# Kernel optimization log

Measured on AMD Instinct MI355X. Metric: run time of the kernel, lower is better.

The kernel has to match this reference:

```python
import jax, jax.numpy as jnp
import numpy as np

KH, KW = 3, 3
C_OUT = 32


def setup_inputs() -> dict:
    key = jax.random.key(0)
    k1, k2, k3 = jax.random.split(key, 3)
    B, H, W, C_IN = 32, 128, 128, 32
    P_DIM = 128
    X = jax.random.normal(k1, (B, H, W, C_IN), dtype=jnp.float32)
    P = jax.random.normal(k2, (B, P_DIM), dtype=jnp.float32)
    # hypernetwork Dense weight: p_dim -> kh*kw*c_in*c_out (no bias, no activation)
    dense_w = jax.random.normal(k3, (P_DIM, KH * KW * C_IN * C_OUT), dtype=jnp.float32) * 0.05
    return {"X": X, "P": P, "dense_w": dense_w}


def _conv_one(x, w):
    # x: [H, W, c_in], w: [kh, kw, c_in, c_out] -> [H, W, c_out], SAME padding, stride 1
    y = jax.lax.conv_general_dilated(
        x[None], w, window_strides=(1, 1), padding="SAME",
        dimension_numbers=("NHWC", "HWIO", "NHWC"))
    return y[0]


def reference(X, P, dense_w):
    B = X.shape[0]
    c_in = X.shape[-1]
    # hypernetwork: per-sample conv kernels
    A = P @ dense_w                              # [B, kh*kw*c_in*c_out]
    Wk = A.reshape(B, KH, KW, c_in, C_OUT)       # [B, kh, kw, c_in, c_out]
    # batched per-sample conv (equivalent to tf.map_fn over conv2d)
    return jax.vmap(_conv_one)(X, Wk)            # [B, H, W, c_out]
```

## Files before the change

kernel.cpp:

```cpp
#include <hip/hip_runtime.h>


#define BATCH 32
#define HDIM 128
#define WDIM 128
#define CIN 32
#define COUT 32
#define PDIM 128
#define KCOLS 9216

typedef _Float16 f16x8 __attribute__((ext_vector_type(8)));
typedef float f32x4 __attribute__((ext_vector_type(4)));

__device__ __forceinline__ f16x8 zero8() {
    f16x8 z;
#pragma unroll
    for (int j = 0; j < 8; ++j) z[j] = (_Float16)0.f;
    return z;
}

__device__ __forceinline__ f16x8 cvt8(f32x4 lo, f32x4 hi) {
    f16x8 o;
#pragma unroll
    for (int j = 0; j < 4; ++j) {
        o[j] = (_Float16)lo[j];
        o[4 + j] = (_Float16)hi[j];
    }
    return o;
}

__global__ __launch_bounds__(256) void hyper_gemm(const float* __restrict__ P,
                                                  const float* __restrict__ Dw,
                                                  unsigned short* __restrict__ WB) {
    const int tid = threadIdx.x;
    const int lane = tid & 63;
    const int cg = blockIdx.x % 144;
    const int bq = blockIdx.x / 144;
    const int col = cg * 64 + lane;
    const int b0 = __builtin_amdgcn_readfirstlane(bq * 16 + (tid >> 6) * 4);
    const float* pb = P + (size_t)b0 * PDIM;

    float acc[4];
#pragma unroll
    for (int j = 0; j < 4; ++j) acc[j] = 0.f;

#pragma unroll 2
    for (int mm = 0; mm < PDIM; mm += 16) {
        float d[16];
#pragma unroll
        for (int u = 0; u < 16; ++u) d[u] = Dw[(size_t)(mm + u) * KCOLS + col];
#pragma unroll
        for (int u = 0; u < 16; ++u) {
#pragma unroll
            for (int j = 0; j < 4; ++j) acc[j] += d[u] * pb[j * PDIM + mm + u];
        }
    }

    const int co = col & 31;
    const int k = col >> 5;
    const int kc = k >> 5;
    const int ci = k & 31;
    const int base =
        ((kc * 2 + (co >> 4)) * 64 + (ci >> 3) * 16 + (co & 15)) * 8 + (ci & 7);
#pragma unroll
    for (int j = 0; j < 4; ++j) {
        _Float16 v = (_Float16)acc[j];
        WB[(size_t)(b0 + j) * KCOLS + base] = __builtin_bit_cast(unsigned short, v);
    }
}

__device__ __forceinline__ f16x8 halo_ld(const f32x4* __restrict__ gp, int px) {
    const bool ok = (unsigned)px < 128u;
    const int p = ok ? px : 0;
    f32x4 lo = gp[p * 8];
    f32x4 hi = gp[p * 8 + 1];
    f16x8 o;
#pragma unroll
    for (int j = 0; j < 4; ++j) {
        o[j] = (_Float16)lo[j];
        o[4 + j] = (_Float16)hi[j];
    }
    if (!ok) o = zero8();
    return o;
}

template <bool TOPG, bool PRE>
__device__ __forceinline__ void compute_group(const char* xsb, int ldsbase,
                                              const f16x8* bfl, float* ybase,
                                              const f32x4* gp, bool gvalid,
                                              int wave, int q, int m16,
                                              f32x4* R, const float* xsrc1) {
    f16x8 hal[3];
    if (gvalid) {
#pragma unroll
        for (int kw = 0; kw < 3; ++kw) hal[kw] = halo_ld(gp, m16 + kw - 1);
    } else {
#pragma unroll
        for (int kw = 0; kw < 3; ++kw) hal[kw] = zero8();
    }

    int va[3];
#pragma unroll
    for (int kw = 0; kw < 3; ++kw) {
        const int px = m16 + kw - 1;
        const int sl = (q ^ (px >> 1)) & 3;
        va[kw] = ldsbase + (wave - 1) * 8192 + px * 64 + sl * 16;
    }

#pragma unroll
    for (int t = 0; t < 8; ++t) {
        if constexpr (PRE) {
            R[2 * t] = *(const f32x4*)(xsrc1 + (size_t)t * WDIM * CIN);
            R[2 * t + 1] = *(const f32x4*)(xsrc1 + (size_t)t * WDIM * CIN + 4);
        }

        f32x4 acc0 = {0.f, 0.f, 0.f, 0.f};
        f32x4 acc1 = {0.f, 0.f, 0.f, 0.f};

#pragma unroll
        for (int kh = 0; kh < 3; ++kh) {
            f16x8 a0, a1, a2;
            const bool use_lds = (kh == 1) || (kh == 0 && (!TOPG || wave != 0)) ||
                                 (kh == 2 && wave != 7);
            if (use_lds) {
                int v0 = va[0] + kh * 8192;
                int v1 = va[1] + kh * 8192;
                int v2 = va[2] + kh * 8192;
                if (t == 0) v0 += (m16 == 0) ? 64 : 0;
                if (t == 7) v2 -= (m16 == 15) ? 64 : 0;
                a0 = *(const f16x8*)(xsb + v0);
                a1 = *(const f16x8*)(xsb + v1);
                a2 = *(const f16x8*)(xsb + v2);
                if (t == 0 && m16 == 0) a0 = zero8();
                if (t == 7 && m16 == 15) a2 = zero8();
            } else {
                a0 = hal[0];
                a1 = hal[1];
                a2 = hal[2];
                if (gvalid && t < 7) {
#pragma unroll
                    for (int kw = 0; kw < 3; ++kw)
                        hal[kw] = halo_ld(gp, (t + 1) * 16 + m16 + kw - 1);
                }
            }
            acc0 = __builtin_amdgcn_mfma_f32_16x16x32_f16(a0, bfl[((kh * 3 + 0) * 2 + 0) * 64], acc0, 0, 0, 0);
            acc1 = __builtin_amdgcn_mfma_f32_16x16x32_f16(a0, bfl[((kh * 3 + 0) * 2 + 1) * 64], acc1, 0, 0, 0);
            acc0 = __builtin_amdgcn_mfma_f32_16x16x32_f16(a1, bfl[((kh * 3 + 1) * 2 + 0) * 64], acc0, 0, 0, 0);
            acc1 = __builtin_amdgcn_mfma_f32_16x16x32_f16(a1, bfl[((kh * 3 + 1) * 2 + 1) * 64], acc1, 0, 0, 0);
            acc0 = __builtin_amdgcn_mfma_f32_16x16x32_f16(a2, bfl[((kh * 3 + 2) * 2 + 0) * 64], acc0, 0, 0, 0);
            acc1 = __builtin_amdgcn_mfma_f32_16x16x32_f16(a2, bfl[((kh * 3 + 2) * 2 + 1) * 64], acc1, 0, 0, 0);
        }

        float* yp = ybase + t * 16 * COUT;
#pragma unroll
        for (int r = 0; r < 4; ++r) {
            yp[r * COUT] = acc0[r];
            yp[r * COUT + 16] = acc1[r];
        }

#pragma unroll
        for (int kw = 0; kw < 3; ++kw) va[kw] += 1024;
    }
}

__global__ __launch_bounds__(512, 2) void conv_fused(const float* __restrict__ X,
                                                     const unsigned short* __restrict__ WB,
                                                     float* __restrict__ Y) {
    __shared__ f16x8 Xs[16 * 512];
    __shared__ f16x8 BFs[KCOLS / 8];
    const int tid = threadIdx.x;

    const int wg = blockIdx.x;
    const int id = (wg & 7) * 32 + (wg >> 3);
    const int b = id >> 3;
    const int hg = id & 7;
    const int r0 = hg * 16;

    const int wave = tid >> 6;
    const int lane = tid & 63;
    const int q = lane >> 4;
    const int m16 = lane & 15;

    {
        const f16x8* wbp = (const f16x8*)(WB + (size_t)b * KCOLS);
        for (int i = tid; i < KCOLS / 8; i += 512) BFs[i] = wbp[i];
    }

    const int px_s = tid >> 2;
    const int q_s = tid & 3;
    const int g_s = px_s * 4 + ((q_s ^ (px_s >> 1)) & 3);
    const float* xsrc = X + (((size_t)b * HDIM + r0) * WDIM + px_s) * CIN + q_s * 8;

#pragma unroll
    for (int r = 0; r < 8; ++r) {
        f32x4 lo = *(const f32x4*)(xsrc + (size_t)r * WDIM * CIN);
        f32x4 hi = *(const f32x4*)(xsrc + (size_t)r * WDIM * CIN + 4);
        Xs[r * 512 + g_s] = cvt8(lo, hi);
    }

    __syncthreads();

    const char* xsb = (const char*)Xs;
    const f16x8* bfl = BFs + lane;
    const f32x4* Xb = (const f32x4*)X + (size_t)b * HDIM * (WDIM * CIN / 4);
    const float* xsrc1 = xsrc + (size_t)8 * WDIM * CIN;
    f32x4 R[16];

    {
        const bool gvalid = (wave == 0) ? (hg != 0) : (wave == 7);
        const int grow = (wave == 0) ? (hg ? r0 - 1 : 0) : (r0 + 8);
        const f32x4* gp = Xb + (size_t)grow * (WDIM * CIN / 4) + q * 2;
        float* yb = Y + (((size_t)b * HDIM + r0 + wave) * WDIM + q * 4) * COUT + m16;
        compute_group<true, true>(xsb, 0, bfl, yb, gp, gvalid, wave, q, m16, R, xsrc1);
    }

#pragma unroll
    for (int r = 0; r < 8; ++r) {
        Xs[(8 + r) * 512 + g_s] = cvt8(R[2 * r], R[2 * r + 1]);
    }
    __syncthreads();

    {
        const bool gvalid = (wave == 7) && (hg != 7);
        const int grow = gvalid ? (r0 + 16) : 0;
        const f32x4* gp = Xb + (size_t)grow * (WDIM * CIN / 4) + q * 2;
        float* yb = Y + (((size_t)b * HDIM + r0 + 8 + wave) * WDIM + q * 4) * COUT + m16;
        compute_group<false, false>(xsb, 8 * 8192, bfl, yb, gp, gvalid, wave, q, m16,
                                    R, xsrc1);
    }
}

extern "C" void kernel_launch(void* const* d_in, const int* in_sizes, int n_in,
                              void* d_out, int out_size, void* d_ws, size_t ws_size,
                              hipStream_t stream) {
    const float* X = (const float*)d_in[0];
    const float* P = (const float*)d_in[1];
    const float* Dw = (const float*)d_in[2];
    float* Y = (float*)d_out;
    (void)ws_size;

    unsigned short* WB = (unsigned short*)d_ws;

    hipLaunchKernelGGL(hyper_gemm, dim3(288), dim3(256), 0, stream, P, Dw, WB);
    hipLaunchKernelGGL(conv_fused, dim3(256), dim3(512), 0, stream, X, WB, Y);
}
```

Baseline: 138.8 us.

## Split conv into 4-row strips with 256-thread blocks and 1024 workgroups

Replaces the 16-row, 512-thread conv kernel, which staged 8 rows, computed, then staged the next 8 with a register prefetch, by a simpler kernel. Each 256-thread workgroup now stages 4 rows in LDS and computes them in one pass, with 1024 workgroups and a target of 3 blocks per CU. The aim is more parallelism and occupancy, plus shorter serial staging per block. In exchange, each block reloads the per-sample weights into LDS, which now happens four times as often, and more halo rows are read from global memory.

```diff
diff --git a/kernel.cpp b/kernel.cpp
--- a/kernel.cpp
+++ b/kernel.cpp
@@ -74,22 +74,65 @@
     const int p = ok ? px : 0;
     f32x4 lo = gp[p * 8];
     f32x4 hi = gp[p * 8 + 1];
-    f16x8 o;
-#pragma unroll
-    for (int j = 0; j < 4; ++j) {
-        o[j] = (_Float16)lo[j];
-        o[4 + j] = (_Float16)hi[j];
-    }
+    f16x8 o = cvt8(lo, hi);
     if (!ok) o = zero8();
     return o;
 }
 
-template <bool TOPG, bool PRE>
-__device__ __forceinline__ void compute_group(const char* xsb, int ldsbase,
-                                              const f16x8* bfl, float* ybase,
-                                              const f32x4* gp, bool gvalid,
-                                              int wave, int q, int m16,
-                                              f32x4* R, const float* xsrc1) {
+__global__ __launch_bounds__(256, 3) void conv_s4(const float* __restrict__ X,
+                                                  const unsigned short* __restrict__ WB,
+                                                  float* __restrict__ Y) {
+    __shared__ f16x8 Xs[4 * 512];
+    __shared__ f16x8 BFs[KCOLS / 8];
+    const int tid = threadIdx.x;
+
+    const int wg = blockIdx.x;
+    const int id = (wg & 7) * 128 + (wg >> 3);
+    const int b = id >> 5;
+    const int hg = id & 31;
+    const int r0 = hg * 4;
+
+    const int wave = tid >> 6;
+    const int lane = tid & 63;
+    const int q = lane >> 4;
+    const int m16 = lane & 15;
+
+    {
+        const f16x8* wbp = (const f16x8*)(WB + (size_t)b * KCOLS);
+#pragma unroll
+        for (int i = 0; i < 5; ++i) {
+            const int idx = tid + i * 256;
+            if (idx < KCOLS / 8) BFs[idx] = wbp[idx];
+        }
+    }
+
+    {
+        const int px_s = tid >> 1;
+        const int qb = (tid & 1) * 2;
+#pragma unroll
+        for (int r = 0; r < 4; ++r) {
+#pragma unroll
+            for (int p = 0; p < 2; ++p) {
+                const int q_s = qb + p;
+                const float* src =
+                    X + (((size_t)b * HDIM + r0 + r) * WDIM + px_s) * CIN + q_s * 8;
+                f32x4 lo = *(const f32x4*)src;
+                f32x4 hi = *(const f32x4*)(src + 4);
+                const int g_s = px_s * 4 + ((q_s ^ (px_s >> 1)) & 3);
+                Xs[r * 512 + g_s] = cvt8(lo, hi);
+            }
+        }
+    }
+    __syncthreads();
+
+    const bool top = (wave == 0);
+    const bool bot = (wave == 3);
+    const bool gvalid = top ? (hg != 0) : (bot ? (hg != 31) : false);
+    const int grow = top ? (hg ? r0 - 1 : 0) : (r0 + 4);
+    const f32x4* gp = (const f32x4*)X +
+                      ((size_t)b * HDIM + (gvalid ? grow : 0)) * (WDIM * CIN / 4) +
+                      q * 2;
+
     f16x8 hal[3];
     if (gvalid) {
 #pragma unroll
@@ -104,24 +147,24 @@
     for (int kw = 0; kw < 3; ++kw) {
         const int px = m16 + kw - 1;
         const int sl = (q ^ (px >> 1)) & 3;
-        va[kw] = ldsbase + (wave - 1) * 8192 + px * 64 + sl * 16;
-    }
+        va[kw] = (wave - 1) * 8192 + px * 64 + sl * 16;
+    }
+
+    const char* xsb = (const char*)Xs;
+    const f16x8* bfl = BFs + lane;
+    const int h = r0 + wave;
+    float* ybase = Y + (((size_t)b * HDIM + h) * WDIM + q * 4) * COUT + m16;
 
 #pragma unroll
     for (int t = 0; t < 8; ++t) {
-        if constexpr (PRE) {
-            R[2 * t] = *(const f32x4*)(xsrc1 + (size_t)t * WDIM * CIN);
-            R[2 * t + 1] = *(const f32x4*)(xsrc1 + (size_t)t * WDIM * CIN + 4);
-        }
-
         f32x4 acc0 = {0.f, 0.f, 0.f, 0.f};
         f32x4 acc1 = {0.f, 0.f, 0.f, 0.f};
 
 #pragma unroll
         for (int kh = 0; kh < 3; ++kh) {
             f16x8 a0, a1, a2;
-            const bool use_lds = (kh == 1) || (kh == 0 && (!TOPG || wave != 0)) ||
-                                 (kh == 2 && wave != 7);
+            const bool use_lds =
+                (kh == 1) || (kh == 0 && wave != 0) || (kh == 2 && wave != 3);
             if (use_lds) {
                 int v0 = va[0] + kh * 8192;
                 int v1 = va[1] + kh * 8192;
@@ -163,73 +206,6 @@
     }
 }
 
-__global__ __launch_bounds__(512, 2) void conv_fused(const float* __restrict__ X,
-                                                     const unsigned short* __restrict__ WB,
-                                                     float* __restrict__ Y) {
-    __shared__ f16x8 Xs[16 * 512];
-    __shared__ f16x8 BFs[KCOLS / 8];
-    const int tid = threadIdx.x;
-
-    const int wg = blockIdx.x;
-    const int id = (wg & 7) * 32 + (wg >> 3);
-    const int b = id >> 3;
-    const int hg = id & 7;
-    const int r0 = hg * 16;
-
-    const int wave = tid >> 6;
-    const int lane = tid & 63;
-    const int q = lane >> 4;
-    const int m16 = lane & 15;
-
-    {
-        const f16x8* wbp = (const f16x8*)(WB + (size_t)b * KCOLS);
-        for (int i = tid; i < KCOLS / 8; i += 512) BFs[i] = wbp[i];
-    }
-
-    const int px_s = tid >> 2;
-    const int q_s = tid & 3;
-    const int g_s = px_s * 4 + ((q_s ^ (px_s >> 1)) & 3);
-    const float* xsrc = X + (((size_t)b * HDIM + r0) * WDIM + px_s) * CIN + q_s * 8;
-
-#pragma unroll
-    for (int r = 0; r < 8; ++r) {
-        f32x4 lo = *(const f32x4*)(xsrc + (size_t)r * WDIM * CIN);
-        f32x4 hi = *(const f32x4*)(xsrc + (size_t)r * WDIM * CIN + 4);
-        Xs[r * 512 + g_s] = cvt8(lo, hi);
-    }
-
-    __syncthreads();
-
-    const char* xsb = (const char*)Xs;
-    const f16x8* bfl = BFs + lane;
-    const f32x4* Xb = (const f32x4*)X + (size_t)b * HDIM * (WDIM * CIN / 4);
-    const float* xsrc1 = xsrc + (size_t)8 * WDIM * CIN;
-    f32x4 R[16];
-
-    {
-        const bool gvalid = (wave == 0) ? (hg != 0) : (wave == 7);
-        const int grow = (wave == 0) ? (hg ? r0 - 1 : 0) : (r0 + 8);
-        const f32x4* gp = Xb + (size_t)grow * (WDIM * CIN / 4) + q * 2;
-        float* yb = Y + (((size_t)b * HDIM + r0 + wave) * WDIM + q * 4) * COUT + m16;
-        compute_group<true, true>(xsb, 0, bfl, yb, gp, gvalid, wave, q, m16, R, xsrc1);
-    }
-
-#pragma unroll
-    for (int r = 0; r < 8; ++r) {
-        Xs[(8 + r) * 512 + g_s] = cvt8(R[2 * r], R[2 * r + 1]);
-    }
-    __syncthreads();
-
-    {
-        const bool gvalid = (wave == 7) && (hg != 7);
-        const int grow = gvalid ? (r0 + 16) : 0;
-        const f32x4* gp = Xb + (size_t)grow * (WDIM * CIN / 4) + q * 2;
-        float* yb = Y + (((size_t)b * HDIM + r0 + 8 + wave) * WDIM + q * 4) * COUT + m16;
-        compute_group<false, false>(xsb, 8 * 8192, bfl, yb, gp, gvalid, wave, q, m16,
-                                    R, xsrc1);
-    }
-}
-
 extern "C" void kernel_launch(void* const* d_in, const int* in_sizes, int n_in,
                               void* d_out, int out_size, void* d_ws, size_t ws_size,
                               hipStream_t stream) {
@@ -242,5 +218,5 @@
     unsigned short* WB = (unsigned short*)d_ws;
 
     hipLaunchKernelGGL(hyper_gemm, dim3(288), dim3(256), 0, stream, P, Dw, WB);
-    hipLaunchKernelGGL(conv_fused, dim3(256), dim3(512), 0, stream, X, WB, Y);
-}
+    hipLaunchKernelGGL(conv_s4, dim3(1024), dim3(256), 0, stream, X, WB, Y);
+}
```

Result: slower. 146.7 us (+5.7%).
